# Performance work log

Hardware: AMD Instinct MI355X
Metric: run time of the kernel (lower is better)

## Reference

```python
import jax, jax.numpy as jnp
import numpy as np

B, T, D, H = 16, 4096, 1024, 32
EPS = 1e-6


def setup_inputs() -> dict:
    key = jax.random.key(0)
    ks = jax.random.split(key, 12)
    inp = {
        'Z_real': jax.random.normal(ks[0], (B, T, D), jnp.float32),
        'Z_imag': jax.random.normal(ks[1], (B, T, D), jnp.float32),
        'mask': jnp.ones((B, T), jnp.float32),
        # psi_mag: Linear(1,H) -> GELU -> Linear(H,1)  (xavier gain 0.1, zero bias)
        'W1m': jax.random.normal(ks[2], (H, 1), jnp.float32) * 0.1,
        'b1m': jnp.zeros((H,), jnp.float32),
        'W2m': jax.random.normal(ks[3], (1, H), jnp.float32) * 0.1,
        'b2m': jnp.zeros((1,), jnp.float32),
        # psi_phase: Linear(2,H) -> GELU -> Linear(H,2)
        'W1p': jax.random.normal(ks[4], (H, 2), jnp.float32) * 0.1,
        'b1p': jnp.zeros((H,), jnp.float32),
        'W2p': jax.random.normal(ks[5], (2, H), jnp.float32) * 0.1,
        'b2p': jnp.zeros((2,), jnp.float32),
        'mag_scale': jnp.float32(0.1),
    }
    return inp


def reference(Z_real, Z_imag, mask, W1m, b1m, W2m, b2m, W1p, b1p, W2p, b2p, mag_scale):
    m = mask[:, :, None]  # (B,T,1)
    count = jnp.clip(jnp.sum(m, axis=1, keepdims=True), 1.0)  # (B,1,1)
    Ar = jnp.sum(Z_real * m, axis=1, keepdims=True) / count   # (B,1,D)
    Ai = jnp.sum(Z_imag * m, axis=1, keepdims=True) / count
    mag = jnp.sqrt(Ar * Ar + Ai * Ai)
    log_mag = jnp.log(mag + EPS)                               # (B,1,D)
    phase_vec = jnp.stack([Ar, Ai], axis=-1) / (mag[..., None] + EPS)  # (B,1,D,2)
    # psi_mag on scalar feature
    h = jax.nn.gelu(log_mag[..., None] @ W1m.T + b1m, approximate=False)  # (B,1,D,H)
    mag_delta = (h @ W2m.T + b2m)[..., 0]                      # (B,1,D)
    log_mag_out = log_mag + mag_scale * mag_delta
    # psi_phase on 2-vector
    hp = jax.nn.gelu(phase_vec @ W1p.T + b1p, approximate=False)  # (B,1,D,H)
    pv = hp @ W2p.T + b2p                                      # (B,1,D,2)
    norm = jnp.maximum(jnp.sqrt(jnp.sum(pv * pv, axis=-1, keepdims=True)), 1e-12)
    pv = pv / norm
    r_out = jnp.exp(log_mag_out)
    A_new_r = r_out * pv[..., 0]
    A_new_i = r_out * pv[..., 1]
    out = jnp.stack([Z_real + A_new_r, Z_imag + A_new_i], axis=0)  # (2,B,T,D)
    return out
```

## Files before the change

kernel.cpp:

```cpp
#include <hip/hip_runtime.h>
#include <math.h>

#define BB 16
#define TT 4096
#define DD 1024
#define HH 32
#define TC1 128
#define NC1 (TT / TC1)
#define TC3 64
#define NC3 (TT / TC3)

static constexpr float kEPS = 1e-6f;

typedef float f32x4 __attribute__((ext_vector_type(4)));

__global__ __launch_bounds__(256) void reduce_kernel(
    const float* __restrict__ zr, const float* __restrict__ zi,
    const float* __restrict__ mask,
    float* __restrict__ partR, float* __restrict__ partI,
    float* __restrict__ cntP) {
  const int c = blockIdx.x;
  const int b = blockIdx.y;
  const int tid = threadIdx.x;
  const int d4 = tid * 4;

  f32x4 accR = (f32x4)(0.f);
  f32x4 accI = (f32x4)(0.f);
  float msum = 0.f;

  const size_t base = ((size_t)b * TT + (size_t)c * TC1) * DD + d4;
  const float* zrp = zr + base;
  const float* zip = zi + base;
  const float* mp = mask + (size_t)b * TT + (size_t)c * TC1;

  #pragma unroll 8
  for (int t = 0; t < TC1; ++t) {
    const float m = mp[t];
    msum += m;
    f32x4 r  = *(const f32x4*)(zrp + (size_t)t * DD);
    f32x4 im = *(const f32x4*)(zip + (size_t)t * DD);
    accR += r * m;
    accI += im * m;
  }

  const size_t po = ((size_t)c * BB + b) * DD + d4;
  *(f32x4*)(partR + po) = accR;
  *(f32x4*)(partI + po) = accI;
  if (tid == 0) cntP[c * BB + b] = msum;
}

__global__ __launch_bounds__(256) void mlp_kernel(
    const float* __restrict__ partR, const float* __restrict__ partI,
    const float* __restrict__ cntP,
    const float* __restrict__ W1m, const float* __restrict__ b1m,
    const float* __restrict__ W2m, const float* __restrict__ b2m,
    const float* __restrict__ W1p, const float* __restrict__ b1p,
    const float* __restrict__ W2p, const float* __restrict__ b2p,
    const float* __restrict__ mag_scale,
    float* __restrict__ anR, float* __restrict__ anI) {
  const int i = blockIdx.x * blockDim.x + threadIdx.x;
  const int b = i >> 10;
  const int d = i & (DD - 1);

  float count = 0.f;
  #pragma unroll
  for (int c = 0; c < NC1; ++c) count += cntP[c * BB + b];
  count = fmaxf(count, 1.0f);

  float sR = 0.f, sI = 0.f;
  #pragma unroll 8
  for (int c = 0; c < NC1; ++c) {
    const size_t po = ((size_t)c * BB + b) * DD + d;
    sR += partR[po];
    sI += partI[po];
  }

  const float Ar = sR / count;
  const float Ai = sI / count;
  const float mag = sqrtf(Ar * Ar + Ai * Ai);
  const float log_mag = logf(mag + kEPS);
  const float inv_me = 1.0f / (mag + kEPS);
  const float pr = Ar * inv_me;
  const float pi = Ai * inv_me;

  float md = b2m[0];
  #pragma unroll
  for (int j = 0; j < HH; ++j) {
    float h = log_mag * W1m[j] + b1m[j];
    h = 0.5f * h * (1.0f + erff(h * 0.70710678118654752440f));
    md += h * W2m[j];
  }
  const float lmo = log_mag + mag_scale[0] * md;

  float pv0 = b2p[0];
  float pv1 = b2p[1];
  #pragma unroll
  for (int j = 0; j < HH; ++j) {
    float hp = pr * W1p[2 * j] + pi * W1p[2 * j + 1] + b1p[j];
    hp = 0.5f * hp * (1.0f + erff(hp * 0.70710678118654752440f));
    pv0 += hp * W2p[j];
    pv1 += hp * W2p[HH + j];
  }
  const float nrm = fmaxf(sqrtf(pv0 * pv0 + pv1 * pv1), 1e-12f);
  const float r_out = expf(lmo);
  anR[i] = r_out * pv0 / nrm;
  anI[i] = r_out * pv1 / nrm;
}

__global__ __launch_bounds__(256) void add_kernel(
    const float* __restrict__ zr, const float* __restrict__ zi,
    const float* __restrict__ anR, const float* __restrict__ anI,
    float* __restrict__ out) {
  const int c = blockIdx.x;
  const int b = blockIdx.y;
  const int tid = threadIdx.x;
  const int d4 = tid * 4;

  const int o = b * DD + d4;
  const f32x4 ar4 = *(const f32x4*)(anR + o);
  const f32x4 ai4 = *(const f32x4*)(anI + o);

  const size_t base = ((size_t)b * TT + (size_t)c * TC3) * DD + d4;
  const float* zrp = zr + base;
  const float* zip = zi + base;
  float* out0 = out + base;
  float* out1 = out + (size_t)BB * TT * DD + base;

  #pragma unroll 8
  for (int t = 0; t < TC3; ++t) {
    const size_t ro = (size_t)t * DD;
    f32x4 r  = *(const f32x4*)(zrp + ro);
    f32x4 im = *(const f32x4*)(zip + ro);
    r += ar4;
    im += ai4;
    *(f32x4*)(out0 + ro) = r;
    *(f32x4*)(out1 + ro) = im;
  }
}

extern "C" void kernel_launch(void* const* d_in, const int* in_sizes, int n_in,
                              void* d_out, int out_size, void* d_ws, size_t ws_size,
                              hipStream_t stream) {
  const float* zr = (const float*)d_in[0];
  const float* zi = (const float*)d_in[1];
  const float* mask = (const float*)d_in[2];
  const float* W1m = (const float*)d_in[3];
  const float* b1m = (const float*)d_in[4];
  const float* W2m = (const float*)d_in[5];
  const float* b2m = (const float*)d_in[6];
  const float* W1p = (const float*)d_in[7];
  const float* b1p = (const float*)d_in[8];
  const float* W2p = (const float*)d_in[9];
  const float* b2p = (const float*)d_in[10];
  const float* mag_scale = (const float*)d_in[11];

  float* ws = (float*)d_ws;
  float* partR = ws;
  float* partI = ws + 524288;
  float* cntP  = ws + 1048576;
  float* anR   = ws + 1049088;
  float* anI   = ws + 1065472;

  dim3 g1(NC1, BB);
  reduce_kernel<<<g1, 256, 0, stream>>>(zr, zi, mask, partR, partI, cntP);

  mlp_kernel<<<BB * DD / 256, 256, 0, stream>>>(
      partR, partI, cntP, W1m, b1m, W2m, b2m, W1p, b1p, W2p, b2p, mag_scale,
      anR, anI);

  dim3 g3(NC3, BB);
  add_kernel<<<g3, 256, 0, stream>>>(zr, zi, anR, anI, (float*)d_out);
}
```

Measured before the change: 329.9 us.

## Fuse MLP into add kernel, enlarge reduce chunks, use nontemporal reversed streaming

Removes the separate MLP kernel and recomputes the per-(b,d) MLP inside each add block from the reduce partials, saving a launch and the intermediate buffer round trip. Doubles the reduce chunk length to halve the partial count. The add loop now uses nontemporal loads/stores and iterates in reverse order to improve cache behaviour. The cost is redundant MLP computation in every time-chunk block, including many erf evaluations.

Result: slower. 622.3 us (+88.6%).

```diff
diff --git a/kernel.cpp b/kernel.cpp
--- a/kernel.cpp
+++ b/kernel.cpp
@@ -5,7 +5,7 @@
 #define TT 4096
 #define DD 1024
 #define HH 32
-#define TC1 128
+#define TC1 256
 #define NC1 (TT / TC1)
 #define TC3 64
 #define NC3 (TT / TC3)
@@ -49,34 +49,13 @@
   if (tid == 0) cntP[c * BB + b] = msum;
 }
 
-__global__ __launch_bounds__(256) void mlp_kernel(
-    const float* __restrict__ partR, const float* __restrict__ partI,
-    const float* __restrict__ cntP,
+__device__ __forceinline__ void mlp_one(
+    float Ar, float Ai,
     const float* __restrict__ W1m, const float* __restrict__ b1m,
     const float* __restrict__ W2m, const float* __restrict__ b2m,
     const float* __restrict__ W1p, const float* __restrict__ b1p,
     const float* __restrict__ W2p, const float* __restrict__ b2p,
-    const float* __restrict__ mag_scale,
-    float* __restrict__ anR, float* __restrict__ anI) {
-  const int i = blockIdx.x * blockDim.x + threadIdx.x;
-  const int b = i >> 10;
-  const int d = i & (DD - 1);
-
-  float count = 0.f;
-  #pragma unroll
-  for (int c = 0; c < NC1; ++c) count += cntP[c * BB + b];
-  count = fmaxf(count, 1.0f);
-
-  float sR = 0.f, sI = 0.f;
-  #pragma unroll 8
-  for (int c = 0; c < NC1; ++c) {
-    const size_t po = ((size_t)c * BB + b) * DD + d;
-    sR += partR[po];
-    sI += partI[po];
-  }
-
-  const float Ar = sR / count;
-  const float Ai = sI / count;
+    float msc, float& anr, float& ani) {
   const float mag = sqrtf(Ar * Ar + Ai * Ai);
   const float log_mag = logf(mag + kEPS);
   const float inv_me = 1.0f / (mag + kEPS);
@@ -90,7 +69,7 @@
     h = 0.5f * h * (1.0f + erff(h * 0.70710678118654752440f));
     md += h * W2m[j];
   }
-  const float lmo = log_mag + mag_scale[0] * md;
+  const float lmo = log_mag + msc * md;
 
   float pv0 = b2p[0];
   float pv1 = b2p[1];
@@ -103,22 +82,51 @@
   }
   const float nrm = fmaxf(sqrtf(pv0 * pv0 + pv1 * pv1), 1e-12f);
   const float r_out = expf(lmo);
-  anR[i] = r_out * pv0 / nrm;
-  anI[i] = r_out * pv1 / nrm;
+  anr = r_out * pv0 / nrm;
+  ani = r_out * pv1 / nrm;
 }
 
 __global__ __launch_bounds__(256) void add_kernel(
     const float* __restrict__ zr, const float* __restrict__ zi,
-    const float* __restrict__ anR, const float* __restrict__ anI,
+    const float* __restrict__ partR, const float* __restrict__ partI,
+    const float* __restrict__ cntP,
+    const float* __restrict__ W1m, const float* __restrict__ b1m,
+    const float* __restrict__ W2m, const float* __restrict__ b2m,
+    const float* __restrict__ W1p, const float* __restrict__ b1p,
+    const float* __restrict__ W2p, const float* __restrict__ b2p,
+    const float* __restrict__ mag_scale,
     float* __restrict__ out) {
   const int c = blockIdx.x;
   const int b = blockIdx.y;
   const int tid = threadIdx.x;
   const int d4 = tid * 4;
 
-  const int o = b * DD + d4;
-  const f32x4 ar4 = *(const f32x4*)(anR + o);
-  const f32x4 ai4 = *(const f32x4*)(anI + o);
+  float count = 0.f;
+  #pragma unroll
+  for (int cc = 0; cc < NC1; ++cc) count += cntP[cc * BB + b];
+  count = fmaxf(count, 1.0f);
+  const float inv_cnt = 1.0f / count;
+
+  f32x4 sR = (f32x4)(0.f);
+  f32x4 sI = (f32x4)(0.f);
+  #pragma unroll
+  for (int cc = 0; cc < NC1; ++cc) {
+    const size_t po = ((size_t)cc * BB + b) * DD + d4;
+    sR += *(const f32x4*)(partR + po);
+    sI += *(const f32x4*)(partI + po);
+  }
+  sR *= inv_cnt;
+  sI *= inv_cnt;
+
+  const float msc = mag_scale[0];
+  f32x4 ar4, ai4;
+  #pragma unroll
+  for (int e = 0; e < 4; ++e) {
+    float anr, ani;
+    mlp_one(sR[e], sI[e], W1m, b1m, W2m, b2m, W1p, b1p, W2p, b2p, msc, anr, ani);
+    ar4[e] = anr;
+    ai4[e] = ani;
+  }
 
   const size_t base = ((size_t)b * TT + (size_t)c * TC3) * DD + d4;
   const float* zrp = zr + base;
@@ -127,14 +135,14 @@
   float* out1 = out + (size_t)BB * TT * DD + base;
 
   #pragma unroll 8
-  for (int t = 0; t < TC3; ++t) {
+  for (int t = TC3 - 1; t >= 0; --t) {
     const size_t ro = (size_t)t * DD;
-    f32x4 r  = *(const f32x4*)(zrp + ro);
-    f32x4 im = *(const f32x4*)(zip + ro);
+    f32x4 r  = __builtin_nontemporal_load((const f32x4*)(zrp + ro));
+    f32x4 im = __builtin_nontemporal_load((const f32x4*)(zip + ro));
     r += ar4;
     im += ai4;
-    *(f32x4*)(out0 + ro) = r;
-    *(f32x4*)(out1 + ro) = im;
+    __builtin_nontemporal_store(r, (f32x4*)(out0 + ro));
+    __builtin_nontemporal_store(im, (f32x4*)(out1 + ro));
   }
 }
 
@@ -156,18 +164,14 @@
 
   float* ws = (float*)d_ws;
   float* partR = ws;
-  float* partI = ws + 524288;
-  float* cntP  = ws + 1048576;
-  float* anR   = ws + 1049088;
-  float* anI   = ws + 1065472;
+  float* partI = ws + NC1 * BB * DD;
+  float* cntP  = ws + 2 * NC1 * BB * DD;
 
   dim3 g1(NC1, BB);
   reduce_kernel<<<g1, 256, 0, stream>>>(zr, zi, mask, partR, partI, cntP);
 
-  mlp_kernel<<<BB * DD / 256, 256, 0, stream>>>(
-      partR, partI, cntP, W1m, b1m, W2m, b2m, W1p, b1p, W2p, b2p, mag_scale,
-      anR, anI);
-
   dim3 g3(NC3, BB);
-  add_kernel<<<g3, 256, 0, stream>>>(zr, zi, anR, anI, (float*)d_out);
+  add_kernel<<<g3, 256, 0, stream>>>(zr, zi, partR, partI, cntP,
+                                     W1m, b1m, W2m, b2m, W1p, b1p, W2p, b2p,
+                                     mag_scale, (float*)d_out);
 }
```
